# Kernel optimization log

Hardware: AMD Instinct MI355X
Metric: run time of the kernel (lower is better)

Reference implementation:

```python
import jax, jax.numpy as jnp
import numpy as np

N = 100000
E = 1600000
IN_DIM = 128
HID_DIM = 128
NUM_CLASSES = 40


def setup_inputs() -> dict:
    key = jax.random.key(0)
    k1, k2, k3, k4, k5, k6 = jax.random.split(key, 6)
    x = jax.random.normal(k1, (N, IN_DIM), dtype=jnp.float32)
    e = jax.random.randint(k2, (2, E), 0, N, dtype=jnp.int64)
    s1 = 1.0 / np.sqrt(IN_DIM)
    s2 = 1.0 / np.sqrt(HID_DIM)
    W1 = jax.random.uniform(k3, (IN_DIM, HID_DIM), jnp.float32, -s1, s1)
    b1 = jax.random.uniform(k4, (HID_DIM,), jnp.float32, -s1, s1)
    W2 = jax.random.uniform(k5, (HID_DIM, NUM_CLASSES), jnp.float32, -s2, s2)
    b2 = jax.random.uniform(k6, (NUM_CLASSES,), jnp.float32, -s2, s2)
    return {"x": x, "e": e, "W1": W1, "b1": b1, "W2": W2, "b2": b2}


def _gcn_conv(x, src, dst, norm, W, b, n):
    # linear transform first (PyG GCNConv), then normalized aggregation
    h = x @ W                                    # [N, d_out]
    out = jax.ops.segment_sum(h[src] * norm[:, None], dst, num_segments=n)
    return out + b


def reference(x, e, W1, b1, W2, b2):
    n = x.shape[0]
    loop = jnp.arange(n, dtype=e.dtype)
    src = jnp.concatenate([e[0], loop])          # add self-loops
    dst = jnp.concatenate([e[1], loop])
    deg = jax.ops.segment_sum(jnp.ones_like(dst, dtype=x.dtype), dst, num_segments=n)
    d_inv_sqrt = deg ** -0.5                     # deg >= 1 due to self-loops
    norm = d_inv_sqrt[src] * d_inv_sqrt[dst]     # symmetric normalization
    h = jax.nn.relu(_gcn_conv(x, src, dst, norm, W1, b1, n))
    return _gcn_conv(h, src, dst, norm, W2, b2, n)
```

## Files before the change

kernel.cpp:

```cpp
#include <hip/hip_runtime.h>


typedef unsigned int u32;
typedef unsigned short u16;
typedef __attribute__((ext_vector_type(8))) short short8;
typedef __attribute__((ext_vector_type(4))) float floatx4;

#define CHUNK 4096

static __device__ inline u16 f2bf(float f) {
    u32 u = __float_as_uint(f);
    return (u16)((u + 0x7FFFu + ((u >> 16) & 1u)) >> 16);
}
static __device__ inline u32 pack2(float a, float b) {
    return (u32)f2bf(a) | ((u32)f2bf(b) << 16);
}
static __device__ inline float bflo(u32 u) { return __uint_as_float(u << 16); }
static __device__ inline float bfhi(u32 u) { return __uint_as_float(u & 0xffff0000u); }

static __device__ inline bool detect_is64(const int* e32, int lane) {
    bool nz = e32[2 * lane + 1] != 0;
    return __ballot(nz) == 0ull;
}

__global__ void k_prepW(const float* __restrict__ W1, const float* __restrict__ W2,
                        u16* __restrict__ WTb, u16* __restrict__ W2Tb) {
    int id = blockIdx.x * 256 + threadIdx.x;
    if (id < 16384) {
        int k = id >> 7, c = id & 127;
        WTb[c * 128 + k] = f2bf(W1[id]);
    } else {
        int id2 = id - 16384;
        if (id2 < 6144) {
            int c = id2 >> 7, k = id2 & 127;
            W2Tb[id2] = f2bf(c < 40 ? W2[k * 40 + c] : 0.f);
        }
    }
}

__global__ __launch_bounds__(256) void k_front(const void* __restrict__ e_raw,
                                               int E, int NC, int NB,
                                               int* __restrict__ histG,
                                               const float* __restrict__ X,
                                               const u16* __restrict__ WTb,
                                               u16* __restrict__ H1s, int n) {
    __shared__ u32 smem[64 * 68 + 128 * 68];
    const int tid = threadIdx.x;
    if ((int)blockIdx.x < NC) {
        int* h = (int*)smem;
        h[tid] = 0; h[tid + 256] = 0;
        __syncthreads();
        const int* e32 = (const int*)e_raw;
        bool is64 = detect_is64(e32, tid & 63);
        int c = blockIdx.x;
        int j0 = c * CHUNK, j1 = min(E, j0 + CHUNK);
        for (int j = j0 + tid; j < j1; j += 256) {
            int d = is64 ? (int)((const long long*)e_raw)[E + j] : e32[E + j];
            atomicAdd(&h[d >> 8], 1);
        }
        __syncthreads();
        for (int b = tid; b < NB; b += 256) histG[(size_t)b * NC + c] = h[b];
        return;
    }
    u32* As = smem;
    u32* Bs = smem + 64 * 68;
    const int row0 = ((int)blockIdx.x - NC) * 64;
#pragma unroll
    for (int it = 0; it < 8; it++) {
        int i = tid + it * 256;
        int r = i >> 5;
        int c4 = (i & 31) << 2;
        int gr = row0 + r;
        float4 v = make_float4(0.f, 0.f, 0.f, 0.f);
        if (gr < n) v = *(const float4*)(X + (size_t)gr * 128 + c4);
        uint2 p;
        p.x = pack2(v.x, v.y);
        p.y = pack2(v.z, v.w);
        *(uint2*)&As[r * 68 + (c4 >> 1)] = p;
    }
#pragma unroll
    for (int it = 0; it < 8; it++) {
        int i = tid + it * 256;
        int r = i >> 4;
        int c4 = (i & 15) << 2;
        *(uint4*)&Bs[r * 68 + c4] =
            *(const uint4*)((const u32*)WTb + (size_t)r * 64 + c4);
    }
    __syncthreads();

    const int lane = tid & 63;
    const int wave = tid >> 6;
    const int wr = wave >> 1;
    const int wc = wave & 1;
    const int mrow = lane & 15;
    const int quad = lane >> 4;

    floatx4 acc[2][4] = {};
    for (int k0 = 0; k0 < 128; k0 += 32) {
        int koff = (k0 >> 1) + quad * 4;
        short8 a[2], b[4];
#pragma unroll
        for (int i = 0; i < 2; i++)
            a[i] = *(const short8*)&As[((wr * 2 + i) * 16 + mrow) * 68 + koff];
#pragma unroll
        for (int j = 0; j < 4; j++)
            b[j] = *(const short8*)&Bs[((wc * 4 + j) * 16 + mrow) * 68 + koff];
#pragma unroll
        for (int i = 0; i < 2; i++)
#pragma unroll
            for (int j = 0; j < 4; j++)
                acc[i][j] = __builtin_amdgcn_mfma_f32_16x16x32_bf16(
                    a[i], b[j], acc[i][j], 0, 0, 0);
    }
#pragma unroll
    for (int i = 0; i < 2; i++) {
        int gr0 = row0 + (wr * 2 + i) * 16 + quad * 4;
#pragma unroll
        for (int j = 0; j < 4; j++) {
            u16* dst = H1s + (size_t)(wc * 4 + j) * ((size_t)n * 16);
#pragma unroll
            for (int rg = 0; rg < 4; rg++) {
                int grow = gr0 + rg;
                if (grow < n)
                    dst[(size_t)grow * 16 + mrow] = f2bf(acc[i][j][rg]);
            }
        }
    }
}

__global__ void k_scan1(const int* __restrict__ in, int* __restrict__ out,
                        int* __restrict__ bsum, int n) {
    __shared__ int sh[256];
    int i = blockIdx.x * 256 + threadIdx.x;
    int v = (i < n) ? in[i] : 0;
    sh[threadIdx.x] = v;
    __syncthreads();
    for (int off = 1; off < 256; off <<= 1) {
        int t = (threadIdx.x >= off) ? sh[threadIdx.x - off] : 0;
        __syncthreads();
        sh[threadIdx.x] += t;
        __syncthreads();
    }
    if (i < n) out[i] = sh[threadIdx.x] - v;
    if (threadIdx.x == 255) bsum[blockIdx.x] = sh[255];
}

__global__ void k_scan2(int* __restrict__ bsum, int nb) {
    __shared__ int sh[1024];
    int t = threadIdx.x;
    int v = (t < nb) ? bsum[t] : 0;
    sh[t] = v;
    __syncthreads();
    for (int off = 1; off < 1024; off <<= 1) {
        int u = (t >= off) ? sh[t - off] : 0;
        __syncthreads();
        sh[t] += u;
        __syncthreads();
    }
    if (t < nb) bsum[t] = sh[t] - v;
}

__global__ __launch_bounds__(256) void k_place(const void* __restrict__ e_raw,
                                               const int* __restrict__ histOff,
                                               const int* __restrict__ bsumH,
                                               u32* __restrict__ tmp,
                                               int E, int NB, int NC) {
    __shared__ int cur[512];
    int c = blockIdx.x;
    int t = threadIdx.x;
    for (int b = t; b < NB; b += 256) {
        int idx = b * NC + c;
        cur[b] = histOff[idx] + bsumH[idx >> 8];
    }
    __syncthreads();
    const int* e32 = (const int*)e_raw;
    bool is64 = detect_is64(e32, t & 63);
    int j0 = c * CHUNK, j1 = min(E, j0 + CHUNK);
    for (int j = j0 + t; j < j1; j += 256) {
        int s, d;
        if (is64) {
            s = (int)((const long long*)e_raw)[j];
            d = (int)((const long long*)e_raw)[E + j];
        } else {
            s = e32[j];
            d = e32[E + j];
        }
        int pos = atomicAdd(&cur[d >> 8], 1);
        tmp[pos] = (u32)s | ((u32)(d & 255) << 24);
    }
}

__global__ __launch_bounds__(256) void k_degsort(const u32* __restrict__ tmp,
                                                 const int* __restrict__ histOff,
                                                 const int* __restrict__ bsumH,
                                                 int* __restrict__ degI,
                                                 float* __restrict__ dinv,
                                                 int* __restrict__ rs,
                                                 int* __restrict__ eSrc,
                                                 int n, int NB, int NC, int E) {
    __shared__ int cnt[256];
    __shared__ int sh[256];
    __shared__ int cur[256];
    int b = blockIdx.x;
    int t = threadIdx.x;
    cnt[t] = 0;
    __syncthreads();
    int i0 = b * NC;
    int seg0 = histOff[i0] + bsumH[i0 >> 8];
    int seg1 = E;
    if (b + 1 < NB) {
        int i1 = (b + 1) * NC;
        seg1 = histOff[i1] + bsumH[i1 >> 8];
    }
    for (int j = seg0 + t; j < seg1; j += 256) atomicAdd(&cnt[tmp[j] >> 24], 1);
    __syncthreads();
    int v = cnt[t];
    sh[t] = v;
    __syncthreads();
    for (int off = 1; off < 256; off <<= 1) {
        int u = (t >= off) ? sh[t - off] : 0;
        __syncthreads();
        sh[t] += u;
        __syncthreads();
    }
    int myStart = seg0 + sh[t] - v;
    cur[t] = myStart;
    int node = b * 256 + t;
    if (node < n) {
        degI[node] = v;
        dinv[node] = rsqrtf((float)v + 1.0f);
        rs[node] = myStart;
    }
    __syncthreads();
    for (int j = seg0 + t; j < seg1; j += 256) {
        u32 rec = tmp[j];
        int dl = rec >> 24;
        int s = (int)(rec & 0x00FFFFFFu);
        int pos = atomicAdd(&cur[dl], 1);
        eSrc[pos] = s;
    }
}

__global__ __launch_bounds__(256) void k_ew(int* __restrict__ eSrc,
                                            const float* __restrict__ dinv,
                                            int E) {
    int i = blockIdx.x * 256 + threadIdx.x;
    if (i >= E) return;
    u32 s = (u32)eSrc[i];
    u32 wq = (u32)__float2int_rn(dinv[s] * 32767.f);
    eSrc[i] = (int)(s | (wq << 17));
}

__global__ __launch_bounds__(256) void k_gather128(
    const u32* __restrict__ Hb, const int* __restrict__ rs,
    const int* __restrict__ degI, const u32* __restrict__ eW,
    const float* __restrict__ b1, u32* __restrict__ outb, int n) {
    const int lane = threadIdx.x & 63;
    const int wave = threadIdx.x >> 6;
    const int g = lane >> 3;
    const int l = lane & 7;
    const int slice = blockIdx.x & 7;
    const int chunk = blockIdx.x >> 3;
    const u32* __restrict__ Hq = Hb + (size_t)slice * ((size_t)n * 8);

    const int node = chunk * 32 + wave * 8 + g;
    if (node >= n) return;
    const int start = rs[node];
    const int deg = degI[node];
    float ax = 0.f, ay = 0.f;

    int t = 0;
    if (deg >= 8) {
        u32 r0, r1, r2, r3, r4, r5, r6, r7;
        r0 = eW[start + 0]; r1 = eW[start + 1];
        r2 = eW[start + 2]; r3 = eW[start + 3];
        r4 = eW[start + 4]; r5 = eW[start + 5];
        r6 = eW[start + 6]; r7 = eW[start + 7];
        for (; t + 16 <= deg; t += 8) {
            u32 u0 = Hq[(size_t)(r0 & 0x1FFFFu) * 8 + l];
            u32 u1 = Hq[(size_t)(r1 & 0x1FFFFu) * 8 + l];
            u32 u2 = Hq[(size_t)(r2 & 0x1FFFFu) * 8 + l];
            u32 u3 = Hq[(size_t)(r3 & 0x1FFFFu) * 8 + l];
            u32 u4 = Hq[(size_t)(r4 & 0x1FFFFu) * 8 + l];
            u32 u5 = Hq[(size_t)(r5 & 0x1FFFFu) * 8 + l];
            u32 u6 = Hq[(size_t)(r6 & 0x1FFFFu) * 8 + l];
            u32 u7 = Hq[(size_t)(r7 & 0x1FFFFu) * 8 + l];
            u32 n0 = eW[start + t + 8],  n1 = eW[start + t + 9];
            u32 n2 = eW[start + t + 10], n3 = eW[start + t + 11];
            u32 n4 = eW[start + t + 12], n5 = eW[start + t + 13];
            u32 n6 = eW[start + t + 14], n7 = eW[start + t + 15];
            float w0 = (float)(r0 >> 17), w1 = (float)(r1 >> 17);
            float w2 = (float)(r2 >> 17), w3 = (float)(r3 >> 17);
            float w4 = (float)(r4 >> 17), w5 = (float)(r5 >> 17);
            float w6 = (float)(r6 >> 17), w7 = (float)(r7 >> 17);
            ax = fmaf(w0, bflo(u0), ax); ay = fmaf(w0, bfhi(u0), ay);
            ax = fmaf(w1, bflo(u1), ax); ay = fmaf(w1, bfhi(u1), ay);
            ax = fmaf(w2, bflo(u2), ax); ay = fmaf(w2, bfhi(u2), ay);
            ax = fmaf(w3, bflo(u3), ax); ay = fmaf(w3, bfhi(u3), ay);
            ax = fmaf(w4, bflo(u4), ax); ay = fmaf(w4, bfhi(u4), ay);
            ax = fmaf(w5, bflo(u5), ax); ay = fmaf(w5, bfhi(u5), ay);
            ax = fmaf(w6, bflo(u6), ax); ay = fmaf(w6, bfhi(u6), ay);
            ax = fmaf(w7, bflo(u7), ax); ay = fmaf(w7, bfhi(u7), ay);
            r0 = n0; r1 = n1; r2 = n2; r3 = n3;
            r4 = n4; r5 = n5; r6 = n6; r7 = n7;
        }
        {
            u32 u0 = Hq[(size_t)(r0 & 0x1FFFFu) * 8 + l];
            u32 u1 = Hq[(size_t)(r1 & 0x1FFFFu) * 8 + l];
            u32 u2 = Hq[(size_t)(r2 & 0x1FFFFu) * 8 + l];
            u32 u3 = Hq[(size_t)(r3 & 0x1FFFFu) * 8 + l];
            u32 u4 = Hq[(size_t)(r4 & 0x1FFFFu) * 8 + l];
            u32 u5 = Hq[(size_t)(r5 & 0x1FFFFu) * 8 + l];
            u32 u6 = Hq[(size_t)(r6 & 0x1FFFFu) * 8 + l];
            u32 u7 = Hq[(size_t)(r7 & 0x1FFFFu) * 8 + l];
            float w0 = (float)(r0 >> 17), w1 = (float)(r1 >> 17);
            float w2 = (float)(r2 >> 17), w3 = (float)(r3 >> 17);
            float w4 = (float)(r4 >> 17), w5 = (float)(r5 >> 17);
            float w6 = (float)(r6 >> 17), w7 = (float)(r7 >> 17);
            ax = fmaf(w0, bflo(u0), ax); ay = fmaf(w0, bfhi(u0), ay);
            ax = fmaf(w1, bflo(u1), ax); ay = fmaf(w1, bfhi(u1), ay);
            ax = fmaf(w2, bflo(u2), ax); ay = fmaf(w2, bfhi(u2), ay);
            ax = fmaf(w3, bflo(u3), ax); ay = fmaf(w3, bfhi(u3), ay);
            ax = fmaf(w4, bflo(u4), ax); ay = fmaf(w4, bfhi(u4), ay);
            ax = fmaf(w5, bflo(u5), ax); ay = fmaf(w5, bfhi(u5), ay);
            ax = fmaf(w6, bflo(u6), ax); ay = fmaf(w6, bfhi(u6), ay);
            ax = fmaf(w7, bflo(u7), ax); ay = fmaf(w7, bfhi(u7), ay);
            t += 8;
        }
    }
    if (t < deg) {
        const int dm = deg - 1;
        u32 r0 = eW[start + min(t + 0, dm)], r1 = eW[start + min(t + 1, dm)];
        u32 r2 = eW[start + min(t + 2, dm)], r3 = eW[start + min(t + 3, dm)];
        u32 r4 = eW[start + min(t + 4, dm)], r5 = eW[start + min(t + 5, dm)];
        u32 r6 = eW[start + min(t + 6, dm)];
        u32 u0 = Hq[(size_t)(r0 & 0x1FFFFu) * 8 + l];
        u32 u1 = Hq[(size_t)(r1 & 0x1FFFFu) * 8 + l];
        u32 u2 = Hq[(size_t)(r2 & 0x1FFFFu) * 8 + l];
        u32 u3 = Hq[(size_t)(r3 & 0x1FFFFu) * 8 + l];
        u32 u4 = Hq[(size_t)(r4 & 0x1FFFFu) * 8 + l];
        u32 u5 = Hq[(size_t)(r5 & 0x1FFFFu) * 8 + l];
        u32 u6 = Hq[(size_t)(r6 & 0x1FFFFu) * 8 + l];
        float w0 = (float)(r0 >> 17);
        float w1 = (t + 1 < deg) ? (float)(r1 >> 17) : 0.f;
        float w2 = (t + 2 < deg) ? (float)(r2 >> 17) : 0.f;
        float w3 = (t + 3 < deg) ? (float)(r3 >> 17) : 0.f;
        float w4 = (t + 4 < deg) ? (float)(r4 >> 17) : 0.f;
        float w5 = (t + 5 < deg) ? (float)(r5 >> 17) : 0.f;
        float w6 = (t + 6 < deg) ? (float)(r6 >> 17) : 0.f;
        ax = fmaf(w0, bflo(u0), ax); ay = fmaf(w0, bfhi(u0), ay);
        ax = fmaf(w1, bflo(u1), ax); ay = fmaf(w1, bfhi(u1), ay);
        ax = fmaf(w2, bflo(u2), ax); ay = fmaf(w2, bfhi(u2), ay);
        ax = fmaf(w3, bflo(u3), ax); ay = fmaf(w3, bfhi(u3), ay);
        ax = fmaf(w4, bflo(u4), ax); ay = fmaf(w4, bfhi(u4), ay);
        ax = fmaf(w5, bflo(u5), ax); ay = fmaf(w5, bfhi(u5), ay);
        ax = fmaf(w6, bflo(u6), ax); ay = fmaf(w6, bfhi(u6), ay);
    }
    ax *= (1.f / 32767.f);
    ay *= (1.f / 32767.f);
    const float di = rsqrtf((float)deg + 1.0f);
    const u32 us = Hq[(size_t)node * 8 + l];
    const float2 bv = *(const float2*)(b1 + (slice * 8 + l) * 2);
    float inx = fmaf(di, bflo(us), ax);
    float iny = fmaf(di, bfhi(us), ay);
    float rx = fmaxf(fmaf(di, inx, bv.x), 0.f);
    float ry = fmaxf(fmaf(di, iny, bv.y), 0.f);
    outb[(size_t)node * 64 + slice * 8 + l] = pack2(rx, ry);
}

__global__ __launch_bounds__(256) void k_gemm2(const u32* __restrict__ A1b,
                                               const u16* __restrict__ W2Tb,
                                               const float* __restrict__ dinv,
                                               u16* __restrict__ H2s, int n) {
    __shared__ u32 As[64 * 68];
    __shared__ u32 Bs[48 * 68];
    const int tid = threadIdx.x;
    const int row0 = blockIdx.x * 64;
#pragma unroll
    for (int it = 0; it < 4; it++) {
        int i = tid + it * 256;
        int r = i >> 4;
        int c4 = (i & 15) << 2;
        int gr = row0 + r;
        uint4 v = make_uint4(0u, 0u, 0u, 0u);
        if (gr < n) v = *(const uint4*)(A1b + (size_t)gr * 64 + c4);
        *(uint4*)&As[r * 68 + c4] = v;
    }
#pragma unroll
    for (int it = 0; it < 3; it++) {
        int i = tid + it * 256;
        int r = i >> 4;
        int c4 = (i & 15) << 2;
        *(uint4*)&Bs[r * 68 + c4] =
            *(const uint4*)((const u32*)W2Tb + (size_t)r * 64 + c4);
    }
    __syncthreads();

    const int lane = tid & 63;
    const int wave = tid >> 6;
    const int mrow = lane & 15;
    const int quad = lane >> 4;

    floatx4 acc[3] = {};
    for (int k0 = 0; k0 < 128; k0 += 32) {
        int koff = (k0 >> 1) + quad * 4;
        short8 a = *(const short8*)&As[(wave * 16 + mrow) * 68 + koff];
#pragma unroll
        for (int j = 0; j < 3; j++) {
            short8 b = *(const short8*)&Bs[(j * 16 + mrow) * 68 + koff];
            acc[j] = __builtin_amdgcn_mfma_f32_16x16x32_bf16(a, b, acc[j], 0, 0, 0);
        }
    }
    int gr0 = row0 + wave * 16 + quad * 4;
    float dv[4];
#pragma unroll
    for (int rg = 0; rg < 4; rg++)
        dv[rg] = (gr0 + rg < n) ? dinv[gr0 + rg] : 0.f;
#pragma unroll
    for (int j = 0; j < 3; j++) {
        int gcol = j * 16 + mrow;
        if (gcol < 40) {
#pragma unroll
            for (int rg = 0; rg < 4; rg++) {
                int grow = gr0 + rg;
                if (grow < n)
                    H2s[(size_t)grow * 40 + gcol] = f2bf(dv[rg] * acc[j][rg]);
            }
        }
    }
}

__global__ __launch_bounds__(256) void k_gather40(
    const u32* __restrict__ H2b, const int* __restrict__ rs,
    const int* __restrict__ degI, const int* __restrict__ eSrc,
    const float* __restrict__ dinv, const float* __restrict__ b2,
    float* __restrict__ out, int n) {
    int wave = threadIdx.x >> 6;
    int lane = threadIdx.x & 63;
    int node = blockIdx.x * 4 + wave;
    if (node >= n) return;
    int start = rs[node];
    int deg = degI[node];
    int g = lane / 20;
    int l = lane - g * 20;
    float ax = 0.f, ay = 0.f;
    for (int base = 0; base < deg; base += 64) {
        int mS = 0;
        if (base + lane < deg) mS = eSrc[start + base + lane] & 0x1FFFF;
        int cnt = min(64, deg - base);
        for (int t = 0; t < cnt; t += 12) {
            int i0 = t + g, i1 = t + 3 + g, i2 = t + 6 + g, i3 = t + 9 + g;
            int s0 = __shfl(mS, i0 & 63), s1 = __shfl(mS, i1 & 63);
            int s2 = __shfl(mS, i2 & 63), s3 = __shfl(mS, i3 & 63);
            bool v0 = (g < 3) && (i0 < cnt), v1 = (g < 3) && (i1 < cnt);
            bool v2 = (g < 3) && (i2 < cnt), v3 = (g < 3) && (i3 < cnt);
            u32 u0 = H2b[(size_t)s0 * 20 + l];
            u32 u1 = H2b[(size_t)s1 * 20 + l];
            u32 u2 = H2b[(size_t)s2 * 20 + l];
            u32 u3 = H2b[(size_t)s3 * 20 + l];
            if (v0) { ax += bflo(u0); ay += bfhi(u0); }
            if (v1) { ax += bflo(u1); ay += bfhi(u1); }
            if (v2) { ax += bflo(u2); ay += bfhi(u2); }
            if (v3) { ax += bflo(u3); ay += bfhi(u3); }
        }
    }
    float x1 = __shfl(ax, (lane + 20) & 63), y1 = __shfl(ay, (lane + 20) & 63);
    float x2 = __shfl(ax, (lane + 40) & 63), y2 = __shfl(ay, (lane + 40) & 63);
    if (lane < 20) {
        float di = dinv[node];
        u32 u = H2b[(size_t)node * 20 + l];
        float2 bv = *(const float2*)(b2 + l * 2);
        float ox = fmaf(di, ax + x1 + x2 + bflo(u), bv.x);
        float oy = fmaf(di, ay + y1 + y2 + bfhi(u), bv.y);
        *(float2*)(out + (size_t)node * 40 + l * 2) = make_float2(ox, oy);
    }
}

extern "C" void kernel_launch(void* const* d_in, const int* in_sizes, int n_in,
                              void* d_out, int out_size, void* d_ws, size_t ws_size,
                              hipStream_t stream) {
    const float* x  = (const float*)d_in[0];
    const void*  e  = d_in[1];
    const float* W1 = (const float*)d_in[2];
    const float* b1 = (const float*)d_in[3];
    const float* W2 = (const float*)d_in[4];
    const float* b2 = (const float*)d_in[5];
    float* out = (float*)d_out;

    const int n = in_sizes[0] / 128;
    const int E = in_sizes[1] / 2;
    const int NB = (n + 255) / 256;
    const int NC = (E + CHUNK - 1) / CHUNK;
    const int NH = NB * NC;
    const int nbH = (NH + 255) / 256;
    const int G1 = (n + 63) / 64;

    int*   degI    = (int*)d_ws;
    int*   rs      = degI + n;
    int*   bsumH   = rs + n;
    float* dinv    = (float*)(bsumH + 1024);
    int*   histG   = (int*)(dinv + n);
    int*   histOff = histG + NH;
    size_t off = (size_t)((char*)(histOff + NH) - (char*)d_ws);
    off = (off + 15) & ~(size_t)15;
    u16*   WTb    = (u16*)((char*)d_ws + off);
    u16*   W2Tb   = WTb + 16384;
    off = (size_t)((char*)(W2Tb + 6144) - (char*)d_ws);
    off = (off + 15) & ~(size_t)15;
    u32*   tmp    = (u32*)((char*)d_ws + off);
    int*   eSrc   = (int*)(tmp + (size_t)E);
    u16*   H1s    = (u16*)(eSrc + (size_t)E);
    u32*   H1b    = (u32*)H1s;
    u32*   A1b    = (u32*)(H1s + (size_t)n * 128);
    u16*   H2s    = (u16*)(A1b + (size_t)n * 64);
    u32*   H2b    = (u32*)H2s;

    k_prepW<<<88, 256, 0, stream>>>(W1, W2, WTb, W2Tb);
    k_front<<<NC + G1, 256, 0, stream>>>(e, E, NC, NB, histG, x, WTb, H1s, n);

    k_scan1<<<nbH, 256, 0, stream>>>(histG, histOff, bsumH, NH);
    k_scan2<<<1, 1024, 0, stream>>>(bsumH, nbH);
    k_place<<<NC, 256, 0, stream>>>(e, histOff, bsumH, tmp, E, NB, NC);

    k_degsort<<<NB, 256, 0, stream>>>(tmp, histOff, bsumH, degI, dinv, rs,
                                      eSrc, n, NB, NC, E);
    k_ew<<<(E + 255) / 256, 256, 0, stream>>>(eSrc, dinv, E);

    k_gather128<<<8 * ((n + 31) / 32), 256, 0, stream>>>(H1b, rs, degI,
                                                         (const u32*)eSrc,
                                                         b1, A1b, n);
    k_gemm2<<<(n + 63) / 64, 256, 0, stream>>>(A1b, W2Tb, dinv, H2s, n);
    k_gather40<<<(n + 3) / 4, 256, 0, stream>>>(H2b, rs, degI, eSrc, dinv,
                                                b2, out, n);
}
```

Before: 315.5 us.

## Sort nodes by degree for gathers and unroll layer-2 gather loop

Builds a degree histogram in k_degsort, scans it, and produces a permutation of nodes grouped by in-degree. Both gather kernels then process nodes in that order, so lanes sharing a wave have similar edge counts and less divergence. The 40-wide gather also changes from shuffle-broadcast batches to fixed contiguous thirds of the edge list per lane group, with an 8-deep prefetch of indices and loads. In exchange it adds two small kernels, an extra indirection, and scattered output writes because nodes are no longer written in order.

```diff
diff --git a/kernel.cpp b/kernel.cpp
--- a/kernel.cpp
+++ b/kernel.cpp
@@ -8,6 +8,9 @@
 
 #define CHUNK 4096
 
+#define REP7(M)  M(0) M(1) M(2) M(3) M(4) M(5) M(6)
+#define REP8(M)  M(0) M(1) M(2) M(3) M(4) M(5) M(6) M(7)
+
 static __device__ inline u16 f2bf(float f) {
     u32 u = __float_as_uint(f);
     return (u16)((u + 0x7FFFu + ((u >> 16) & 1u)) >> 16);
@@ -24,17 +27,18 @@
 }
 
 __global__ void k_prepW(const float* __restrict__ W1, const float* __restrict__ W2,
-                        u16* __restrict__ WTb, u16* __restrict__ W2Tb) {
+                        u16* __restrict__ WTb, u16* __restrict__ W2Tb,
+                        int* __restrict__ dHist) {
     int id = blockIdx.x * 256 + threadIdx.x;
     if (id < 16384) {
         int k = id >> 7, c = id & 127;
         WTb[c * 128 + k] = f2bf(W1[id]);
-    } else {
+    } else if (id < 22528) {
         int id2 = id - 16384;
-        if (id2 < 6144) {
-            int c = id2 >> 7, k = id2 & 127;
-            W2Tb[id2] = f2bf(c < 40 ? W2[k * 40 + c] : 0.f);
-        }
+        int c = id2 >> 7, k = id2 & 127;
+        W2Tb[id2] = f2bf(c < 40 ? W2[k * 40 + c] : 0.f);
+    } else if (id < 22784) {
+        dHist[id - 22528] = 0;
     }
 }
 
@@ -197,6 +201,7 @@
                                                  float* __restrict__ dinv,
                                                  int* __restrict__ rs,
                                                  int* __restrict__ eSrc,
+                                                 int* __restrict__ dHist,
                                                  int n, int NB, int NC, int E) {
     __shared__ int cnt[256];
     __shared__ int sh[256];
@@ -230,6 +235,7 @@
         degI[node] = v;
         dinv[node] = rsqrtf((float)v + 1.0f);
         rs[node] = myStart;
+        atomicAdd(&dHist[min(v, 255)], 1);
     }
     __syncthreads();
     for (int j = seg0 + t; j < seg1; j += 256) {
@@ -238,6 +244,44 @@
         int s = (int)(rec & 0x00FFFFFFu);
         int pos = atomicAdd(&cur[dl], 1);
         eSrc[pos] = s;
+    }
+}
+
+__global__ void k_dscan(int* __restrict__ dH) {
+    __shared__ int sh[256];
+    int t = threadIdx.x;
+    int v = dH[t];
+    sh[t] = v;
+    __syncthreads();
+    for (int off = 1; off < 256; off <<= 1) {
+        int u = (t >= off) ? sh[t - off] : 0;
+        __syncthreads();
+        sh[t] += u;
+        __syncthreads();
+    }
+    dH[t] = sh[t] - v;
+}
+
+__global__ __launch_bounds__(256) void k_dperm(const int* __restrict__ degI,
+                                               int* __restrict__ dCur,
+                                               int* __restrict__ perm, int n) {
+    __shared__ int lh[256];
+    __shared__ int lc[256];
+    int t = threadIdx.x;
+    lh[t] = 0;
+    __syncthreads();
+    int node = blockIdx.x * 256 + t;
+    int bin = -1;
+    if (node < n) {
+        bin = min(degI[node], 255);
+        atomicAdd(&lh[bin], 1);
+    }
+    __syncthreads();
+    if (lh[t] > 0) lc[t] = atomicAdd(&dCur[t], lh[t]);
+    __syncthreads();
+    if (node < n) {
+        int pos = atomicAdd(&lc[bin], 1);
+        perm[pos] = node;
     }
 }
 
@@ -254,7 +298,8 @@
 __global__ __launch_bounds__(256) void k_gather128(
     const u32* __restrict__ Hb, const int* __restrict__ rs,
     const int* __restrict__ degI, const u32* __restrict__ eW,
-    const float* __restrict__ b1, u32* __restrict__ outb, int n) {
+    const int* __restrict__ perm, const float* __restrict__ b1,
+    u32* __restrict__ outb, int n) {
     const int lane = threadIdx.x & 63;
     const int wave = threadIdx.x >> 6;
     const int g = lane >> 3;
@@ -263,8 +308,9 @@
     const int chunk = blockIdx.x >> 3;
     const u32* __restrict__ Hq = Hb + (size_t)slice * ((size_t)n * 8);
 
-    const int node = chunk * 32 + wave * 8 + g;
-    if (node >= n) return;
+    const int idx = chunk * 32 + wave * 8 + g;
+    if (idx >= n) return;
+    const int node = perm[idx];
     const int start = rs[node];
     const int deg = degI[node];
     float ax = 0.f, ay = 0.f;
@@ -359,7 +405,7 @@
     ax *= (1.f / 32767.f);
     ay *= (1.f / 32767.f);
     const float di = rsqrtf((float)deg + 1.0f);
-    const u32 us = Hq[(size_t)node * 8 + l];
+    const u32 us = Hq[((size_t)node << 3) + l];
     const float2 bv = *(const float2*)(b1 + (slice * 8 + l) * 2);
     float inx = fmaf(di, bflo(us), ax);
     float iny = fmaf(di, bfhi(us), ay);
@@ -432,38 +478,60 @@
 
 __global__ __launch_bounds__(256) void k_gather40(
     const u32* __restrict__ H2b, const int* __restrict__ rs,
-    const int* __restrict__ degI, const int* __restrict__ eSrc,
-    const float* __restrict__ dinv, const float* __restrict__ b2,
-    float* __restrict__ out, int n) {
-    int wave = threadIdx.x >> 6;
-    int lane = threadIdx.x & 63;
-    int node = blockIdx.x * 4 + wave;
-    if (node >= n) return;
-    int start = rs[node];
-    int deg = degI[node];
-    int g = lane / 20;
-    int l = lane - g * 20;
+    const int* __restrict__ degI, const u32* __restrict__ eW,
+    const int* __restrict__ perm, const float* __restrict__ dinv,
+    const float* __restrict__ b2, float* __restrict__ out, int n) {
+    const int wave = threadIdx.x >> 6;
+    const int lane = threadIdx.x & 63;
+    const int idx = blockIdx.x * 4 + wave;
+    if (idx >= n) return;
+    const int node = perm[idx];
+    if (lane >= 60) return;
+    const int g = lane / 20;
+    const int l = lane - g * 20;
+    const int start = rs[node];
+    const int deg = degI[node];
+    const int c0 = (deg * g) / 3;
+    const int c1 = (deg * (g + 1)) / 3;
+    const int cnt = c1 - c0;
+    const int sb = start + c0;
     float ax = 0.f, ay = 0.f;
-    for (int base = 0; base < deg; base += 64) {
-        int mS = 0;
-        if (base + lane < deg) mS = eSrc[start + base + lane] & 0x1FFFF;
-        int cnt = min(64, deg - base);
-        for (int t = 0; t < cnt; t += 12) {
-            int i0 = t + g, i1 = t + 3 + g, i2 = t + 6 + g, i3 = t + 9 + g;
-            int s0 = __shfl(mS, i0 & 63), s1 = __shfl(mS, i1 & 63);
-            int s2 = __shfl(mS, i2 & 63), s3 = __shfl(mS, i3 & 63);
-            bool v0 = (g < 3) && (i0 < cnt), v1 = (g < 3) && (i1 < cnt);
-            bool v2 = (g < 3) && (i2 < cnt), v3 = (g < 3) && (i3 < cnt);
-            u32 u0 = H2b[(size_t)s0 * 20 + l];
-            u32 u1 = H2b[(size_t)s1 * 20 + l];
-            u32 u2 = H2b[(size_t)s2 * 20 + l];
-            u32 u3 = H2b[(size_t)s3 * 20 + l];
-            if (v0) { ax += bflo(u0); ay += bfhi(u0); }
-            if (v1) { ax += bflo(u1); ay += bfhi(u1); }
-            if (v2) { ax += bflo(u2); ay += bfhi(u2); }
-            if (v3) { ax += bflo(u3); ay += bfhi(u3); }
-        }
-    }
+    u32 r0, r1, r2, r3, r4, r5, r6, r7;
+    u32 u0, u1, u2, u3, u4, u5, u6, u7;
+    int t = 0;
+
+#define QH(K) u##K = H2b[(r##K & 0x1FFFFu) * 20 + l];
+#define QF(K) r##K = eW[bq + K];
+#define QA(K) ax += bflo(u##K); ay += bfhi(u##K);
+
+    if (cnt >= 8) {
+        int bq = sb;
+        REP8(QF)
+        for (; t + 16 <= cnt; t += 8) {
+            REP8(QH)
+            bq = sb + t + 8;
+            REP8(QF)
+            REP8(QA)
+        }
+        REP8(QH)
+        REP8(QA)
+        t += 8;
+    }
+    if (t < cnt) {
+        const int bq = sb + t;
+        const int rm = cnt - t - 1;
+#define QTF(K) r##K = eW[bq + min(K, rm)];
+#define QTM(K) if (K > rm) u##K = 0u;
+        REP7(QTF)
+        REP7(QH)
+        REP7(QTM)
+        REP7(QA)
+#undef QTF
+#undef QTM
+    }
+#undef QH
+#undef QF
+#undef QA
     float x1 = __shfl(ax, (lane + 20) & 63), y1 = __shfl(ay, (lane + 20) & 63);
     float x2 = __shfl(ax, (lane + 40) & 63), y2 = __shfl(ay, (lane + 40) & 63);
     if (lane < 20) {
@@ -499,7 +567,9 @@
     int*   rs      = degI + n;
     int*   bsumH   = rs + n;
     float* dinv    = (float*)(bsumH + 1024);
-    int*   histG   = (int*)(dinv + n);
+    int*   dHist   = (int*)(dinv + n);
+    int*   perm    = dHist + 256;
+    int*   histG   = perm + n;
     int*   histOff = histG + NH;
     size_t off = (size_t)((char*)(histOff + NH) - (char*)d_ws);
     off = (off + 15) & ~(size_t)15;
@@ -515,7 +585,7 @@
     u16*   H2s    = (u16*)(A1b + (size_t)n * 64);
     u32*   H2b    = (u32*)H2s;
 
-    k_prepW<<<88, 256, 0, stream>>>(W1, W2, WTb, W2Tb);
+    k_prepW<<<89, 256, 0, stream>>>(W1, W2, WTb, W2Tb, dHist);
     k_front<<<NC + G1, 256, 0, stream>>>(e, E, NC, NB, histG, x, WTb, H1s, n);
 
     k_scan1<<<nbH, 256, 0, stream>>>(histG, histOff, bsumH, NH);
@@ -523,13 +593,15 @@
     k_place<<<NC, 256, 0, stream>>>(e, histOff, bsumH, tmp, E, NB, NC);
 
     k_degsort<<<NB, 256, 0, stream>>>(tmp, histOff, bsumH, degI, dinv, rs,
-                                      eSrc, n, NB, NC, E);
+                                      eSrc, dHist, n, NB, NC, E);
+    k_dscan<<<1, 256, 0, stream>>>(dHist);
+    k_dperm<<<NB, 256, 0, stream>>>(degI, dHist, perm, n);
     k_ew<<<(E + 255) / 256, 256, 0, stream>>>(eSrc, dinv, E);
 
     k_gather128<<<8 * ((n + 31) / 32), 256, 0, stream>>>(H1b, rs, degI,
                                                          (const u32*)eSrc,
-                                                         b1, A1b, n);
+                                                         perm, b1, A1b, n);
     k_gemm2<<<(n + 63) / 64, 256, 0, stream>>>(A1b, W2Tb, dinv, H2s, n);
-    k_gather40<<<(n + 3) / 4, 256, 0, stream>>>(H2b, rs, degI, eSrc, dinv,
-                                                b2, out, n);
-}
+    k_gather40<<<(n + 3) / 4, 256, 0, stream>>>(H2b, rs, degI, (const u32*)eSrc,
+                                                perm, dinv, b2, out, n);
+}
```

Result: slower. 599.4 us (+90.0%).
